# Performance work log

Measured on AMD Instinct MI355X. Metric: run time of the kernel, lower is better.

## Reference

```python
import jax, jax.numpy as jnp
import numpy as np

NB_HEADS = 12


def setup_inputs() -> dict:
    key = jax.random.key(0)
    ks = jax.random.split(key, 6)
    B, S, D, H = 4, 1024, 768, NB_HEADS
    x = jax.random.normal(ks[0], (B, S, D), dtype=jnp.float32)
    Wqkv = jax.random.normal(ks[1], (D, 3 * D), dtype=jnp.float32) * 0.02
    bqkv = jnp.zeros((3 * D,), dtype=jnp.float32)
    Wl = jax.random.normal(ks[2], (H, H), dtype=jnp.float32) * 0.3
    bl = jnp.zeros((H,), dtype=jnp.float32)
    Ww = jax.random.normal(ks[3], (H, H), dtype=jnp.float32) * 0.3
    bw = jnp.zeros((H,), dtype=jnp.float32)
    Wproj = jax.random.normal(ks[4], (D, D), dtype=jnp.float32) * 0.02
    bproj = jnp.zeros((D,), dtype=jnp.float32)
    return {"x": x, "Wqkv": Wqkv, "bqkv": bqkv, "Wl": Wl, "bl": bl,
            "Ww": Ww, "bw": bw, "Wproj": Wproj, "bproj": bproj}


def reference(x, Wqkv, bqkv, Wl, bl, Ww, bw, Wproj, bproj):
    B, S, D = x.shape
    H = NB_HEADS
    dh = D // H
    scale = dh ** (-0.5)
    # qkv projection: [B,S,3D] -> [3,B,H,S,dh]
    qkv = (x @ Wqkv + bqkv).reshape(B, S, 3, H, dh).transpose(2, 0, 3, 1, 4)
    q, k, v = qkv[0] * scale, qkv[1], qkv[2]
    # raw attention logits [B,H,S,S]
    attn = jnp.einsum('bhqd,bhkd->bhqk', q, k)
    # pre-softmax talking-heads mix across head dim (Dense over heads)
    attn = jnp.einsum('bhqk,hg->bgqk', attn, Wl) + bl[None, :, None, None]
    attn = jax.nn.softmax(attn, axis=-1)
    # post-softmax talking-heads mix
    attn = jnp.einsum('bhqk,hg->bgqk', attn, Ww) + bw[None, :, None, None]
    # attention-weighted values -> [B,S,D]
    out = jnp.einsum('bhqk,bhkd->bqhd', attn, v).reshape(B, S, D)
    return out @ Wproj + bproj
```

## Files before the change

### kernel.cpp

```cpp
#include <hip/hip_runtime.h>
#include <cstdint>

#define BB 4
#define SS 1024
#define DD 768
#define HH 12
#define DH 64

typedef unsigned short u16;
typedef unsigned int   u32;
typedef __attribute__((ext_vector_type(8))) short bf16x8;
typedef __attribute__((ext_vector_type(4))) float f32x4;

__device__ __forceinline__ u16 f2bf(float f) {
    u32 u = __float_as_uint(f);
    u += 0x7fffu + ((u >> 16) & 1u);
    return (u16)(u >> 16);
}
__device__ __forceinline__ float b2f(u32 lo16) {
    return __uint_as_float(lo16 << 16);
}

#if __has_builtin(__builtin_amdgcn_cvt_pk_bf16_f32)
__device__ __forceinline__ u32 pack2(float a, float b) {
    auto r = __builtin_amdgcn_cvt_pk_bf16_f32(a, b);
    u32 v; __builtin_memcpy(&v, &r, 4); return v;
}
#else
__device__ __forceinline__ u32 pack2(float a, float b) {
    return (u32)f2bf(a) | ((u32)f2bf(b) << 16);
}
#endif

#define ASYNC16(gp, lp) __builtin_amdgcn_global_load_lds( \
    (const __attribute__((address_space(1))) void*)(gp),  \
    (__attribute__((address_space(3))) void*)(lp), 16, 0, 0)

template<int BM_, int BN_, class Epi>
__device__ __forceinline__ void mfma_gemm(
    const u16* __restrict__ A, const u16* __restrict__ B,
    int K, int lda, int ldb, int m0, int n0, const Epi& epi)
{
    constexpr int MI = BM_ / 32;
    constexpr int NJ = BN_ / 32;
    __shared__ u16 Alds[BM_ * 32];
    __shared__ u16 Blds[BN_ * 32];

    const int tid  = threadIdx.x;
    const int wave = tid >> 6;
    const int lane = tid & 63;
    const int wr = wave >> 1, wc = wave & 1;

    const int ar = lane >> 2;
    const int ac = (lane & 3) * 8;

    f32x4 acc[MI][NJ] = {};

    for (int k0 = 0; k0 < K; k0 += 32) {
        __syncthreads();
#pragma unroll
        for (int j = 0; j < BM_ / 64; ++j) {
            const int rb = wave * (BM_ / 4) + j * 16;
            ASYNC16(A + (size_t)(m0 + rb + ar) * lda + k0 + ac, &Alds[rb * 32]);
        }
#pragma unroll
        for (int j = 0; j < BN_ / 64; ++j) {
            const int rb = wave * (BN_ / 4) + j * 16;
            ASYNC16(B + (size_t)(n0 + rb + ar) * ldb + k0 + ac, &Blds[rb * 32]);
        }
        __syncthreads();

        bf16x8 af[MI], bfr[NJ];
#pragma unroll
        for (int mi = 0; mi < MI; ++mi)
            af[mi] = *(const bf16x8*)&Alds[(wr * (BM_ / 2) + mi * 16 + (lane & 15)) * 32 + (lane >> 4) * 8];
#pragma unroll
        for (int nj = 0; nj < NJ; ++nj)
            bfr[nj] = *(const bf16x8*)&Blds[(wc * (BN_ / 2) + nj * 16 + (lane & 15)) * 32 + (lane >> 4) * 8];
#pragma unroll
        for (int mi = 0; mi < MI; ++mi)
#pragma unroll
            for (int nj = 0; nj < NJ; ++nj)
                acc[mi][nj] = __builtin_amdgcn_mfma_f32_16x16x32_bf16(
                    af[mi], bfr[nj], acc[mi][nj], 0, 0, 0);
    }

#pragma unroll
    for (int mi = 0; mi < MI; ++mi)
#pragma unroll
        for (int nj = 0; nj < NJ; ++nj)
#pragma unroll
            for (int r = 0; r < 4; ++r)
                epi(m0 + wr * (BM_ / 2) + mi * 16 + (lane >> 4) * 4 + r,
                    n0 + wc * (BN_ / 2) + nj * 16 + (lane & 15),
                    acc[mi][nj][r]);
}

#define CPAD 136

__global__ __launch_bounds__(256) void qkv_gemm_kernel(
    const u16* __restrict__ xb, const u16* __restrict__ Wt,
    const float* __restrict__ bias,
    u16* __restrict__ qb, u16* __restrict__ kb, u16* __restrict__ vb)
{
    __shared__ u16 Alds[128 * 32];
    __shared__ u16 Blds[128 * 32];
    __shared__ u16 Clds[128 * CPAD];

    const int tid  = threadIdx.x;
    const int wave = tid >> 6;
    const int lane = tid & 63;
    const int wr = wave >> 1, wc = wave & 1;
    const int ar = lane >> 2;
    const int ac = (lane & 3) * 8;
    const int m0 = blockIdx.y * 128, n0 = blockIdx.x * 128;

    f32x4 acc[4][4] = {};

    for (int k0 = 0; k0 < DD; k0 += 32) {
        __syncthreads();
#pragma unroll
        for (int j = 0; j < 2; ++j) {
            const int rb = wave * 32 + j * 16;
            ASYNC16(xb + (size_t)(m0 + rb + ar) * DD + k0 + ac, &Alds[rb * 32]);
            ASYNC16(Wt + (size_t)(n0 + rb + ar) * DD + k0 + ac, &Blds[rb * 32]);
        }
        __syncthreads();

        bf16x8 af[4], bfr[4];
#pragma unroll
        for (int mi = 0; mi < 4; ++mi)
            af[mi] = *(const bf16x8*)&Alds[(wr * 64 + mi * 16 + (lane & 15)) * 32 + (lane >> 4) * 8];
#pragma unroll
        for (int nj = 0; nj < 4; ++nj)
            bfr[nj] = *(const bf16x8*)&Blds[(wc * 64 + nj * 16 + (lane & 15)) * 32 + (lane >> 4) * 8];
#pragma unroll
        for (int mi = 0; mi < 4; ++mi)
#pragma unroll
            for (int nj = 0; nj < 4; ++nj)
                acc[mi][nj] = __builtin_amdgcn_mfma_f32_16x16x32_bf16(
                    af[mi], bfr[nj], acc[mi][nj], 0, 0, 0);
    }

    const int c  = n0 / DD;
    const int w0 = n0 - c * DD;
    const int hA = w0 >> 6;
    const float qs = (c == 0) ? 0.125f : 1.0f;
#pragma unroll
    for (int mi = 0; mi < 4; ++mi)
#pragma unroll
        for (int nj = 0; nj < 4; ++nj)
#pragma unroll
            for (int r = 0; r < 4; ++r) {
                const int row = wr * 64 + mi * 16 + (lane >> 4) * 4 + r;
                const int col = wc * 64 + nj * 16 + (lane & 15);
                Clds[row * CPAD + col] = f2bf((acc[mi][nj][r] + bias[n0 + col]) * qs);
            }
    __syncthreads();

    u16* const dst = (c == 0) ? qb : (c == 1) ? kb : vb;
    const int b = m0 >> 10;
#pragma unroll
    for (int j = 0; j < 8; ++j) {
        const int idx = j * 256 + tid;
        const int row = idx >> 4, u4 = idx & 15;
        const int half = u4 >> 3, d8 = u4 & 7;
        const int h = hA + half;
        const int s = (m0 + row) & 1023;
        const uint4 v = *(const uint4*)&Clds[row * CPAD + half * 64 + d8 * 8];
        *(uint4*)&dst[(((size_t)(b * HH + h) << 10) + s) * DH + d8 * 8] = v;
    }
}

__global__ __launch_bounds__(256) void vtrans_kernel(
    const u16* __restrict__ vb, u16* __restrict__ vt)
{
    __shared__ u16 t[64 * 72];
    const int tid = threadIdx.x;
    const int bh = blockIdx.y;
    const int s0 = blockIdx.x * 64;
    const u16* src = vb + ((size_t)bh << 16) + (size_t)s0 * DH;

#pragma unroll
    for (int j = 0; j < 2; ++j) {
        const int idx = j * 256 + tid;
        const int row = idx >> 3, u4 = idx & 7;
        *(uint4*)&t[row * 72 + u4 * 8] = *(const uint4*)&src[row * DH + u4 * 8];
    }
    __syncthreads();

#pragma unroll
    for (int j = 0; j < 2; ++j) {
        const int idx = j * 256 + tid;
        const int d = idx >> 3, u4 = idx & 7;
        u16 tmp[8];
#pragma unroll
        for (int i = 0; i < 8; ++i) tmp[i] = t[(u4 * 8 + i) * 72 + d];
        *(uint4*)&vt[((size_t)bh * DH + d) * SS + s0 + u4 * 8] = *(const uint4*)tmp;
    }
}

__global__ __launch_bounds__(256) void qk_gemm_kernel(
    const u16* __restrict__ qb, const u16* __restrict__ kb,
    u16* __restrict__ attn, int bh0)
{
    __shared__ u16 Alds[128 * 32];
    __shared__ u16 Blds[128 * 32];
    __shared__ u16 Clds[128 * CPAD];

    const int tid  = threadIdx.x;
    const int wave = tid >> 6;
    const int lane = tid & 63;
    const int wr = wave >> 1, wc = wave & 1;
    const int ar = lane >> 2;
    const int ac = (lane & 3) * 8;
    const int m0 = blockIdx.y * 128, n0 = blockIdx.x * 128;

    const int bhL = blockIdx.z;
    const u16* A = qb + (size_t)(bh0 + bhL) * SS * DH;
    const u16* B = kb + (size_t)(bh0 + bhL) * SS * DH;
    u16* C = attn + (size_t)bhL * SS * SS;

    f32x4 acc[4][4] = {};

#pragma unroll
    for (int k0 = 0; k0 < DH; k0 += 32) {
        __syncthreads();
#pragma unroll
        for (int j = 0; j < 2; ++j) {
            const int rb = wave * 32 + j * 16;
            ASYNC16(A + (size_t)(m0 + rb + ar) * DH + k0 + ac, &Alds[rb * 32]);
            ASYNC16(B + (size_t)(n0 + rb + ar) * DH + k0 + ac, &Blds[rb * 32]);
        }
        __syncthreads();

        bf16x8 af[4], bfr[4];
#pragma unroll
        for (int mi = 0; mi < 4; ++mi)
            af[mi] = *(const bf16x8*)&Alds[(wr * 64 + mi * 16 + (lane & 15)) * 32 + (lane >> 4) * 8];
#pragma unroll
        for (int nj = 0; nj < 4; ++nj)
            bfr[nj] = *(const bf16x8*)&Blds[(wc * 64 + nj * 16 + (lane & 15)) * 32 + (lane >> 4) * 8];
#pragma unroll
        for (int mi = 0; mi < 4; ++mi)
#pragma unroll
            for (int nj = 0; nj < 4; ++nj)
                acc[mi][nj] = __builtin_amdgcn_mfma_f32_16x16x32_bf16(
                    af[mi], bfr[nj], acc[mi][nj], 0, 0, 0);
    }

#pragma unroll
    for (int mi = 0; mi < 4; ++mi)
#pragma unroll
        for (int nj = 0; nj < 4; ++nj)
#pragma unroll
            for (int r = 0; r < 4; ++r) {
                const int row = wr * 64 + mi * 16 + (lane >> 4) * 4 + r;
                const int col = wc * 64 + nj * 16 + (lane & 15);
                Clds[row * CPAD + col] = f2bf(acc[mi][nj][r]);
            }
    __syncthreads();

#pragma unroll
    for (int j = 0; j < 8; ++j) {
        const int idx = j * 256 + tid;
        const int row = idx >> 4, u4 = idx & 15;
        *(uint4*)&C[(size_t)(m0 + row) * SS + n0 + u4 * 8] =
            *(const uint4*)&Clds[row * CPAD + u4 * 8];
    }
}

__global__ __launch_bounds__(256) void pv_gemm_kernel(
    const u16* __restrict__ attn2, const u16* __restrict__ vt,
    u16* __restrict__ ctx, int bh0)
{
    const int bhL = blockIdx.z;
    const int bh = bh0 + bhL;
    const int b = bh / HH, h = bh % HH;
    const u16* A = attn2 + (size_t)bhL * SS * SS;
    const u16* B = vt + (size_t)bh * DH * SS;
    u16* C = ctx + (size_t)b * SS * DD + h * DH;
    struct Epi {
        u16* C;
        __device__ void operator()(int m, int n, float v) const {
            C[(size_t)m * DD + n] = f2bf(v);
        }
    } epi{C};
    mfma_gemm<64, 64>(A, B, SS, SS, SS, blockIdx.y * 64, 0, epi);
}

__global__ __launch_bounds__(256) void proj_gemm_kernel(
    const u16* __restrict__ ctx, const u16* __restrict__ Wt,
    const float* __restrict__ bias, float* __restrict__ out)
{
    struct Epi {
        float* out; const float* bias;
        __device__ void operator()(int m, int n, float v) const {
            out[(size_t)m * DD + n] = v + bias[n];
        }
    } epi{out, bias};
    mfma_gemm<128, 64>(ctx, Wt, DD, DD, DD, blockIdx.y * 128, blockIdx.x * 64, epi);
}

__global__ __launch_bounds__(256) void mix_softmax_kernel(
    const u16* __restrict__ attn, u16* __restrict__ attn2,
    const float* __restrict__ Wl, const float* __restrict__ bl,
    const float* __restrict__ Ww, const float* __restrict__ bw)
{
    __shared__ u16 buf[HH][SS];
    __shared__ float invden[HH];

    const int tid  = threadIdx.x;
    const int wave = tid >> 6;
    const int lane = tid & 63;
    const int bL = blockIdx.x >> 10;
    const int qi = blockIdx.x & (SS - 1);
    const size_t gbase = ((size_t)bL * HH * SS + qi) * SS + tid * 4;
    const int kc = tid * 4;

#pragma unroll
    for (int h = 0; h < HH; ++h)
        *(uint2*)&buf[h][kc] = *(const uint2*)&attn[gbase + (size_t)h * SS * SS];

    {
        float4 vin[HH];
#pragma unroll
        for (int h = 0; h < HH; ++h) {
            const uint2 u = *(const uint2*)&buf[h][kc];
            vin[h].x = b2f(u.x & 0xffff); vin[h].y = b2f(u.x >> 16);
            vin[h].z = b2f(u.y & 0xffff); vin[h].w = b2f(u.y >> 16);
        }
#pragma unroll
        for (int g = 0; g < HH; ++g) {
            float4 s = {bl[g], bl[g], bl[g], bl[g]};
#pragma unroll
            for (int h = 0; h < HH; ++h) {
                const float w = Wl[h * HH + g];
                s.x += vin[h].x * w; s.y += vin[h].y * w;
                s.z += vin[h].z * w; s.w += vin[h].w * w;
            }
            uint2 p;
            p.x = pack2(s.x, s.y); p.y = pack2(s.z, s.w);
            *(uint2*)&buf[g][kc] = p;
        }
    }
    __syncthreads();

#pragma unroll
    for (int rep = 0; rep < 3; ++rep) {
        const int g = rep * 4 + wave;
        float4 v[4];
#pragma unroll
        for (int j = 0; j < 4; ++j) {
            const uint2 u = *(const uint2*)&buf[g][lane * 4 + j * 256];
            v[j].x = b2f(u.x & 0xffff); v[j].y = b2f(u.x >> 16);
            v[j].z = b2f(u.y & 0xffff); v[j].w = b2f(u.y >> 16);
        }

        float ps = 0.f;
#pragma unroll
        for (int j = 0; j < 4; ++j) {
            v[j].x = __expf(v[j].x); v[j].y = __expf(v[j].y);
            v[j].z = __expf(v[j].z); v[j].w = __expf(v[j].w);
            ps += (v[j].x + v[j].y) + (v[j].z + v[j].w);
        }
#pragma unroll
        for (int off = 32; off; off >>= 1) ps += __shfl_xor(ps, off);

#pragma unroll
        for (int j = 0; j < 4; ++j) {
            uint2 p;
            p.x = pack2(v[j].x, v[j].y); p.y = pack2(v[j].z, v[j].w);
            *(uint2*)&buf[g][lane * 4 + j * 256] = p;
        }
        if (lane == 0) invden[g] = 1.0f / ps;
    }
    __syncthreads();

    {
        float4 vin[HH];
#pragma unroll
        for (int h = 0; h < HH; ++h) {
            const uint2 u = *(const uint2*)&buf[h][kc];
            const float inv = invden[h];
            vin[h].x = b2f(u.x & 0xffff) * inv; vin[h].y = b2f(u.x >> 16) * inv;
            vin[h].z = b2f(u.y & 0xffff) * inv; vin[h].w = b2f(u.y >> 16) * inv;
        }
#pragma unroll
        for (int g = 0; g < HH; ++g) {
            float4 s = {bw[g], bw[g], bw[g], bw[g]};
#pragma unroll
            for (int h = 0; h < HH; ++h) {
                const float w = Ww[h * HH + g];
                s.x += vin[h].x * w; s.y += vin[h].y * w;
                s.z += vin[h].z * w; s.w += vin[h].w * w;
            }
            uint2 p;
            p.x = pack2(s.x, s.y); p.y = pack2(s.z, s.w);
            *(uint2*)&attn2[gbase + (size_t)g * SS * SS] = p;
        }
    }
}


__global__ __launch_bounds__(256) void cvt_bf16_kernel(
    const float* __restrict__ in, u16* __restrict__ out, int n8)
{
    const int i = blockIdx.x * 256 + threadIdx.x;
    if (i >= n8) return;
    const float4 a = ((const float4*)in)[i * 2];
    const float4 b = ((const float4*)in)[i * 2 + 1];
    uint4 p;
    p.x = pack2(a.x, a.y); p.y = pack2(a.z, a.w);
    p.z = pack2(b.x, b.y); p.w = pack2(b.z, b.w);
    ((uint4*)out)[i] = p;
}

__global__ __launch_bounds__(256) void cvt_transpose_kernel(
    const float* __restrict__ in, u16* __restrict__ out, int R, int C)
{
    __shared__ float t[32][33];
    const int c0 = blockIdx.x * 32, r0 = blockIdx.y * 32;
    const int tr = threadIdx.x >> 3;
    const int tc = (threadIdx.x & 7) * 4;
    const float4 v = *(const float4*)&in[(size_t)(r0 + tr) * C + c0 + tc];
    t[tc + 0][tr] = v.x; t[tc + 1][tr] = v.y;
    t[tc + 2][tr] = v.z; t[tc + 3][tr] = v.w;
    __syncthreads();
    uint2 p;
    p.x = pack2(t[tr][tc + 0], t[tr][tc + 1]);
    p.y = pack2(t[tr][tc + 2], t[tr][tc + 3]);
    *(uint2*)&out[(size_t)(c0 + tr) * R + r0 + tc] = p;
}

extern "C" void kernel_launch(void* const* d_in, const int* in_sizes, int n_in,
                              void* d_out, int out_size, void* d_ws, size_t ws_size,
                              hipStream_t stream)
{
    const float* x     = (const float*)d_in[0];
    const float* Wqkv  = (const float*)d_in[1];
    const float* bqkv  = (const float*)d_in[2];
    const float* Wl    = (const float*)d_in[3];
    const float* bl    = (const float*)d_in[4];
    const float* Ww    = (const float*)d_in[5];
    const float* bw    = (const float*)d_in[6];
    const float* Wproj = (const float*)d_in[7];
    const float* bproj = (const float*)d_in[8];
    float* out = (float*)d_out;

    const size_t N_XB  = (size_t)BB * SS * DD;
    const size_t N_QB  = (size_t)BB * HH * SS * DH;
    const size_t N_WT  = (size_t)DD * 3 * DD;
    const size_t N_WP  = (size_t)DD * DD;
    const size_t N_AT1 = (size_t)HH * SS * SS;

    u16* xb  = (u16*)d_ws;
    u16* qb  = xb  + N_XB;
    u16* kb  = qb  + N_QB;
    u16* vb  = kb  + N_QB;
    u16* vt  = vb  + N_QB;
    u16* ctx = vt  + N_QB;
    u16* Wqkv_t = ctx + N_XB;
    u16* Wproj_t = Wqkv_t + N_WT;
    u16* attn = Wproj_t + N_WP;

    const size_t fixed_bytes = (size_t)(N_XB * 2 + N_QB * 4 + N_WT + N_WP) * 2;
    int b_per = BB;
    while (b_per > 1 &&
           fixed_bytes + (size_t)b_per * N_AT1 * 2 * 2 > ws_size)
        b_per >>= 1;
    const int n_iter = BB / b_per;
    u16* attn2 = attn + (size_t)b_per * N_AT1;

    const dim3 blk(256);

    cvt_bf16_kernel<<<dim3((N_XB / 8 + 255) / 256), blk, 0, stream>>>(x, xb, (int)(N_XB / 8));
    cvt_transpose_kernel<<<dim3(3 * DD / 32, DD / 32), blk, 0, stream>>>(Wqkv, Wqkv_t, DD, 3 * DD);
    cvt_transpose_kernel<<<dim3(DD / 32, DD / 32), blk, 0, stream>>>(Wproj, Wproj_t, DD, DD);

    qkv_gemm_kernel<<<dim3(3 * DD / 128, BB * SS / 128), blk, 0, stream>>>(
        xb, Wqkv_t, bqkv, qb, kb, vb);
    vtrans_kernel<<<dim3(SS / 64, BB * HH), blk, 0, stream>>>(vb, vt);

    for (int it = 0; it < n_iter; ++it) {
        const int bh0 = it * b_per * HH;
        qk_gemm_kernel<<<dim3(SS / 128, SS / 128, b_per * HH), blk, 0, stream>>>(
            qb, kb, attn, bh0);
        mix_softmax_kernel<<<dim3(b_per * SS), blk, 0, stream>>>(
            attn, attn2, Wl, bl, Ww, bw);
        pv_gemm_kernel<<<dim3(1, SS / 64, b_per * HH), blk, 0, stream>>>(
            attn2, vt, ctx, bh0);
    }

    proj_gemm_kernel<<<dim3(DD / 64, BB * SS / 128), blk, 0, stream>>>(
        ctx, Wproj_t, bproj, out);
}
```

Baseline: 232.5 us.

## Use MFMA for talking-heads mixes and fold softmax normalization into weights

The two 12x12 head-mixing steps in the fused mix/softmax kernel now run as 16x16x32 bf16 MFMA instructions instead of scalar FMA loops. Exponentials are kept in registers and computed with exp2 on log2e-prescaled weights. The per-head softmax denominators are folded into the post-mix weight matrix, which removes a full LDS read/write pass. LDS rows are padded to reduce bank conflicts, at the cost of padding zeros in the MFMA operands, extra cross-lane shuffles and bf16 rounding of the scaled weights.

```diff
diff --git a/kernel.cpp b/kernel.cpp
--- a/kernel.cpp
+++ b/kernel.cpp
@@ -19,6 +19,10 @@
 }
 __device__ __forceinline__ float b2f(u32 lo16) {
     return __uint_as_float(lo16 << 16);
+}
+
+__device__ __forceinline__ float fast_exp2(float x) {
+    return __builtin_amdgcn_exp2f(x);
 }
 
 #if __has_builtin(__builtin_amdgcn_cvt_pk_bf16_f32)
@@ -302,17 +306,22 @@
     mfma_gemm<128, 64>(ctx, Wt, DD, DD, DD, blockIdx.y * 128, blockIdx.x * 64, epi);
 }
 
+#define BSTRIDE 1028
+
 __global__ __launch_bounds__(256) void mix_softmax_kernel(
     const u16* __restrict__ attn, u16* __restrict__ attn2,
     const float* __restrict__ Wl, const float* __restrict__ bl,
     const float* __restrict__ Ww, const float* __restrict__ bw)
 {
-    __shared__ u16 buf[HH][SS];
-    __shared__ float invden[HH];
+    __shared__ u16 buf[HH * BSTRIDE];
+    __shared__ float wsum[4][16];
+    __shared__ float invd[16];
 
     const int tid  = threadIdx.x;
     const int wave = tid >> 6;
     const int lane = tid & 63;
+    const int u    = lane >> 4;
+    const int ln   = lane & 15;
     const int bL = blockIdx.x >> 10;
     const int qi = blockIdx.x & (SS - 1);
     const size_t gbase = ((size_t)bL * HH * SS + qi) * SS + tid * 4;
@@ -320,86 +329,113 @@
 
 #pragma unroll
     for (int h = 0; h < HH; ++h)
-        *(uint2*)&buf[h][kc] = *(const uint2*)&attn[gbase + (size_t)h * SS * SS];
-
+        *(uint2*)&buf[h * BSTRIDE + kc] = *(const uint2*)&attn[gbase + (size_t)h * SS * SS];
+
+    bf16x8 a1;
     {
-        float4 vin[HH];
-#pragma unroll
-        for (int h = 0; h < HH; ++h) {
-            const uint2 u = *(const uint2*)&buf[h][kc];
-            vin[h].x = b2f(u.x & 0xffff); vin[h].y = b2f(u.x >> 16);
-            vin[h].z = b2f(u.y & 0xffff); vin[h].w = b2f(u.y >> 16);
-        }
-#pragma unroll
-        for (int g = 0; g < HH; ++g) {
-            float4 s = {bl[g], bl[g], bl[g], bl[g]};
-#pragma unroll
-            for (int h = 0; h < HH; ++h) {
-                const float w = Wl[h * HH + g];
-                s.x += vin[h].x * w; s.y += vin[h].y * w;
-                s.z += vin[h].z * w; s.w += vin[h].w * w;
-            }
-            uint2 p;
-            p.x = pack2(s.x, s.y); p.y = pack2(s.z, s.w);
-            *(uint2*)&buf[g][kc] = p;
-        }
-    }
-    __syncthreads();
-
-#pragma unroll
-    for (int rep = 0; rep < 3; ++rep) {
-        const int g = rep * 4 + wave;
-        float4 v[4];
-#pragma unroll
-        for (int j = 0; j < 4; ++j) {
-            const uint2 u = *(const uint2*)&buf[g][lane * 4 + j * 256];
-            v[j].x = b2f(u.x & 0xffff); v[j].y = b2f(u.x >> 16);
-            v[j].z = b2f(u.y & 0xffff); v[j].w = b2f(u.y >> 16);
-        }
-
-        float ps = 0.f;
-#pragma unroll
-        for (int j = 0; j < 4; ++j) {
-            v[j].x = __expf(v[j].x); v[j].y = __expf(v[j].y);
-            v[j].z = __expf(v[j].z); v[j].w = __expf(v[j].w);
-            ps += (v[j].x + v[j].y) + (v[j].z + v[j].w);
-        }
-#pragma unroll
-        for (int off = 32; off; off >>= 1) ps += __shfl_xor(ps, off);
-
-#pragma unroll
-        for (int j = 0; j < 4; ++j) {
-            uint2 p;
-            p.x = pack2(v[j].x, v[j].y); p.y = pack2(v[j].z, v[j].w);
-            *(uint2*)&buf[g][lane * 4 + j * 256] = p;
-        }
-        if (lane == 0) invden[g] = 1.0f / ps;
-    }
-    __syncthreads();
-
+        u16 t[8];
+#pragma unroll
+        for (int j = 0; j < 8; ++j) {
+            const int k = u * 8 + j;
+            t[j] = (k < HH && ln < HH) ? f2bf(Wl[k * HH + ln] * 1.44269504f) : (u16)0;
+        }
+        __builtin_memcpy(&a1, t, 16);
+    }
+    f32x4 c1 = {0.f, 0.f, 0.f, 0.f};
+#pragma unroll
+    for (int r = 0; r < 4; ++r) {
+        const int g = u * 4 + r;
+        c1[r] = (g < HH) ? bl[g] * 1.44269504f : 0.f;
+    }
+
+    __syncthreads();
+
+    const int posbase = wave * 256;
+
+    u32 plo[16], phi[16];
+    float part[4] = {0.f, 0.f, 0.f, 0.f};
+
+#pragma unroll
+    for (int mi = 0; mi < 16; ++mi) {
+        const int pos = posbase + mi * 16 + ln;
+        u16 t[8];
+#pragma unroll
+        for (int j = 0; j < 8; ++j) {
+            const int k = u * 8 + j;
+            t[j] = (k < HH) ? buf[k * BSTRIDE + pos] : (u16)0;
+        }
+        bf16x8 bfrag; __builtin_memcpy(&bfrag, t, 16);
+        f32x4 d = __builtin_amdgcn_mfma_f32_16x16x32_bf16(a1, bfrag, c1, 0, 0, 0);
+        const float e0 = fast_exp2(d[0]);
+        const float e1 = fast_exp2(d[1]);
+        const float e2 = fast_exp2(d[2]);
+        const float e3 = fast_exp2(d[3]);
+        part[0] += e0; part[1] += e1; part[2] += e2; part[3] += e3;
+        plo[mi] = pack2(e0, e1);
+        phi[mi] = pack2(e2, e3);
+    }
+
+#pragma unroll
+    for (int off = 1; off < 16; off <<= 1) {
+#pragma unroll
+        for (int r = 0; r < 4; ++r) part[r] += __shfl_xor(part[r], off);
+    }
+    if (ln == 0) {
+#pragma unroll
+        for (int r = 0; r < 4; ++r) wsum[wave][u * 4 + r] = part[r];
+    }
+    __syncthreads();
+    if (tid < 16)
+        invd[tid] = 1.f / (wsum[0][tid] + wsum[1][tid] + wsum[2][tid] + wsum[3][tid]);
+    __syncthreads();
+
+    bf16x8 a2;
     {
-        float4 vin[HH];
-#pragma unroll
-        for (int h = 0; h < HH; ++h) {
-            const uint2 u = *(const uint2*)&buf[h][kc];
-            const float inv = invden[h];
-            vin[h].x = b2f(u.x & 0xffff) * inv; vin[h].y = b2f(u.x >> 16) * inv;
-            vin[h].z = b2f(u.y & 0xffff) * inv; vin[h].w = b2f(u.y >> 16) * inv;
-        }
-#pragma unroll
-        for (int g = 0; g < HH; ++g) {
-            float4 s = {bw[g], bw[g], bw[g], bw[g]};
-#pragma unroll
-            for (int h = 0; h < HH; ++h) {
-                const float w = Ww[h * HH + g];
-                s.x += vin[h].x * w; s.y += vin[h].y * w;
-                s.z += vin[h].z * w; s.w += vin[h].w * w;
-            }
-            uint2 p;
-            p.x = pack2(s.x, s.y); p.y = pack2(s.z, s.w);
-            *(uint2*)&attn2[gbase + (size_t)g * SS * SS] = p;
-        }
-    }
+        u16 t[8];
+#pragma unroll
+        for (int j = 0; j < 8; ++j) {
+            const int k = u * 8 + j;
+            t[j] = (k < HH && ln < HH) ? f2bf(Ww[k * HH + ln] * invd[k]) : (u16)0;
+        }
+        __builtin_memcpy(&a2, t, 16);
+    }
+    f32x4 c2 = {0.f, 0.f, 0.f, 0.f};
+#pragma unroll
+    for (int r = 0; r < 4; ++r) {
+        const int g = u * 4 + r;
+        c2[r] = (g < HH) ? bw[g] : 0.f;
+    }
+
+    const int srcA = ln + ((u == 1) ? 32 : 16);
+#pragma unroll
+    for (int mi = 0; mi < 16; ++mi) {
+        const u32 wlo = plo[mi], whi = phi[mi];
+        const u32 slo = (u32)__shfl((int)wlo, srcA);
+        const u32 shi = (u32)__shfl((int)whi, srcA);
+        u32 wv[4];
+        wv[0] = (u == 0) ? wlo : ((u == 1) ? slo : 0u);
+        wv[1] = (u == 0) ? whi : ((u == 1) ? shi : 0u);
+        wv[2] = (u == 0) ? slo : 0u;
+        wv[3] = (u == 0) ? shi : 0u;
+        bf16x8 b2; __builtin_memcpy(&b2, wv, 16);
+        f32x4 d = __builtin_amdgcn_mfma_f32_16x16x32_bf16(a2, b2, c2, 0, 0, 0);
+
+        const int pos = posbase + mi * 16 + ln;
+        const u32 p01 = pack2(d[0], d[1]);
+        const u32 p23 = pack2(d[2], d[3]);
+        if (u < 3) {
+            buf[(u * 4 + 0) * BSTRIDE + pos] = (u16)p01;
+            buf[(u * 4 + 1) * BSTRIDE + pos] = (u16)(p01 >> 16);
+            buf[(u * 4 + 2) * BSTRIDE + pos] = (u16)p23;
+            buf[(u * 4 + 3) * BSTRIDE + pos] = (u16)(p23 >> 16);
+        }
+    }
+    __syncthreads();
+
+#pragma unroll
+    for (int g = 0; g < HH; ++g)
+        *(uint2*)&attn2[gbase + (size_t)g * SS * SS] =
+            *(const uint2*)&buf[g * BSTRIDE + kc];
 }
 
 
```

Result: slower. 255.9 us (+10.1%).

## Fuse QK GEMM with pre-softmax head mix and exp, MFMA post-mix

Applied to the files above, without the earlier changes.

Replaces the QK GEMM plus mix/softmax kernels with two kernels. The first computes all 12 heads' logits per 16x16 tile directly from global memory, applies the Wl head mix and exp2, writes head-interleaved exp values (padded to 16), and emits partial denominators. The second sums the partials, folds 1/denominator into Ww, and applies the post-softmax mix as a small MFMA before writing attn2. This removes one full round trip of the logits tensor, at the cost of a padded Pbuf layout, uncached direct global loads of Q/K, and strided 2-byte scattered stores in the second kernel.

```diff
diff --git a/kernel.cpp b/kernel.cpp
--- a/kernel.cpp
+++ b/kernel.cpp
@@ -19,6 +19,10 @@
 }
 __device__ __forceinline__ float b2f(u32 lo16) {
     return __uint_as_float(lo16 << 16);
+}
+
+__device__ __forceinline__ float fast_exp2(float x) {
+    return __builtin_amdgcn_exp2f(x);
 }
 
 #if __has_builtin(__builtin_amdgcn_cvt_pk_bf16_f32)
@@ -200,73 +204,132 @@
     }
 }
 
-__global__ __launch_bounds__(256) void qk_gemm_kernel(
+__global__ __launch_bounds__(256) void qkmix_kernel(
     const u16* __restrict__ qb, const u16* __restrict__ kb,
-    u16* __restrict__ attn, int bh0)
-{
-    __shared__ u16 Alds[128 * 32];
-    __shared__ u16 Blds[128 * 32];
-    __shared__ u16 Clds[128 * CPAD];
-
+    const float* __restrict__ Wl, const float* __restrict__ bl,
+    u16* __restrict__ Pbuf, float* __restrict__ den_part, int bh0)
+{
     const int tid  = threadIdx.x;
     const int wave = tid >> 6;
     const int lane = tid & 63;
-    const int wr = wave >> 1, wc = wave & 1;
-    const int ar = lane >> 2;
-    const int ac = (lane & 3) * 8;
-    const int m0 = blockIdx.y * 128, n0 = blockIdx.x * 128;
-
-    const int bhL = blockIdx.z;
-    const u16* A = qb + (size_t)(bh0 + bhL) * SS * DH;
-    const u16* B = kb + (size_t)(bh0 + bhL) * SS * DH;
-    u16* C = attn + (size_t)bhL * SS * SS;
-
-    f32x4 acc[4][4] = {};
-
-#pragma unroll
-    for (int k0 = 0; k0 < DH; k0 += 32) {
-        __syncthreads();
-#pragma unroll
-        for (int j = 0; j < 2; ++j) {
-            const int rb = wave * 32 + j * 16;
-            ASYNC16(A + (size_t)(m0 + rb + ar) * DH + k0 + ac, &Alds[rb * 32]);
-            ASYNC16(B + (size_t)(n0 + rb + ar) * DH + k0 + ac, &Blds[rb * 32]);
-        }
-        __syncthreads();
-
-        bf16x8 af[4], bfr[4];
-#pragma unroll
-        for (int mi = 0; mi < 4; ++mi)
-            af[mi] = *(const bf16x8*)&Alds[(wr * 64 + mi * 16 + (lane & 15)) * 32 + (lane >> 4) * 8];
-#pragma unroll
-        for (int nj = 0; nj < 4; ++nj)
-            bfr[nj] = *(const bf16x8*)&Blds[(wc * 64 + nj * 16 + (lane & 15)) * 32 + (lane >> 4) * 8];
-#pragma unroll
-        for (int mi = 0; mi < 4; ++mi)
-#pragma unroll
-            for (int nj = 0; nj < 4; ++nj)
-                acc[mi][nj] = __builtin_amdgcn_mfma_f32_16x16x32_bf16(
-                    af[mi], bfr[nj], acc[mi][nj], 0, 0, 0);
-    }
-
-#pragma unroll
-    for (int mi = 0; mi < 4; ++mi)
-#pragma unroll
-        for (int nj = 0; nj < 4; ++nj)
-#pragma unroll
-            for (int r = 0; r < 4; ++r) {
-                const int row = wr * 64 + mi * 16 + (lane >> 4) * 4 + r;
-                const int col = wc * 64 + nj * 16 + (lane & 15);
-                Clds[row * CPAD + col] = f2bf(acc[mi][nj][r]);
+    const int u    = lane >> 4;
+    const int ln   = lane & 15;
+    const int kr = blockIdx.x;
+    const int q0 = blockIdx.y * 16;
+    const int bL = blockIdx.z;
+
+    f32x4 dacc[HH] = {};
+
+    for (int kit = 0; kit < 4; ++kit) {
+        const int kc = kr * 256 + kit * 64 + wave * 16;
+        f32x4 acc[HH] = {};
+#pragma unroll
+        for (int h = 0; h < HH; ++h) {
+            const size_t hp = (size_t)(bh0 + bL * HH + h) << 16;
+#pragma unroll
+            for (int ks = 0; ks < 2; ++ks) {
+                const bf16x8 a = *(const bf16x8*)&qb[hp + (size_t)(q0 + ln) * DH + ks * 32 + u * 8];
+                const bf16x8 b = *(const bf16x8*)&kb[hp + (size_t)(kc + ln) * DH + ks * 32 + u * 8];
+                acc[h] = __builtin_amdgcn_mfma_f32_16x16x32_bf16(a, b, acc[h], 0, 0, 0);
             }
+        }
+#pragma unroll
+        for (int r = 0; r < 4; ++r) {
+            float m[HH];
+#pragma unroll
+            for (int g = 0; g < HH; ++g) {
+                float s = bl[g];
+#pragma unroll
+                for (int h = 0; h < HH; ++h) s += acc[h][r] * Wl[h * HH + g];
+                m[g] = fast_exp2(s * 1.44269504f);
+                dacc[g][r] += m[g];
+            }
+            u16* dst = Pbuf + ((size_t)(bL * SS + q0 + u * 4 + r) * SS + kc + ln) * 16;
+            uint4 pa; uint2 pb;
+            pa.x = pack2(m[0], m[1]);  pa.y = pack2(m[2], m[3]);
+            pa.z = pack2(m[4], m[5]);  pa.w = pack2(m[6], m[7]);
+            pb.x = pack2(m[8], m[9]);  pb.y = pack2(m[10], m[11]);
+            *(uint4*)dst = pa;
+            *(uint2*)(dst + 8) = pb;
+        }
+    }
+
+#pragma unroll
+    for (int off = 1; off < 16; off <<= 1)
+#pragma unroll
+        for (int g = 0; g < HH; ++g) {
+            dacc[g][0] += __shfl_xor(dacc[g][0], off);
+            dacc[g][1] += __shfl_xor(dacc[g][1], off);
+            dacc[g][2] += __shfl_xor(dacc[g][2], off);
+            dacc[g][3] += __shfl_xor(dacc[g][3], off);
+        }
+    if (ln == 0) {
+        const size_t dbase = ((size_t)(kr * 4 + wave) * gridDim.z + bL) * (SS * 16);
+#pragma unroll
+        for (int r = 0; r < 4; ++r) {
+            float* dp = den_part + dbase + (size_t)(q0 + u * 4 + r) * 16;
+            float4 v0, v1, v2;
+            v0.x = dacc[0][r]; v0.y = dacc[1][r]; v0.z = dacc[2][r];  v0.w = dacc[3][r];
+            v1.x = dacc[4][r]; v1.y = dacc[5][r]; v1.z = dacc[6][r];  v1.w = dacc[7][r];
+            v2.x = dacc[8][r]; v2.y = dacc[9][r]; v2.z = dacc[10][r]; v2.w = dacc[11][r];
+            *(float4*)dp = v0; *(float4*)(dp + 4) = v1; *(float4*)(dp + 8) = v2;
+        }
+    }
+}
+
+__global__ __launch_bounds__(256) void mix2_kernel(
+    const u16* __restrict__ Pbuf, const float* __restrict__ den_part,
+    const float* __restrict__ Ww, const float* __restrict__ bw,
+    u16* __restrict__ attn2, int nbz)
+{
+    __shared__ float denS[16];
+    const int tid  = threadIdx.x;
+    const int wave = tid >> 6;
+    const int lane = tid & 63;
+    const int u    = lane >> 4;
+    const int ln   = lane & 15;
+    const int bL = blockIdx.x >> 10;
+    const int q  = blockIdx.x & (SS - 1);
+
+    if (tid < 16) {
+        float s = 0.f;
+#pragma unroll
+        for (int p = 0; p < 16; ++p)
+            s += den_part[((size_t)p * nbz + bL) * (SS * 16) + q * 16 + tid];
+        denS[tid] = 1.0f / s;
+    }
     __syncthreads();
 
-#pragma unroll
-    for (int j = 0; j < 8; ++j) {
-        const int idx = j * 256 + tid;
-        const int row = idx >> 4, u4 = idx & 15;
-        *(uint4*)&C[(size_t)(m0 + row) * SS + n0 + u4 * 8] =
-            *(const uint4*)&Clds[row * CPAD + u4 * 8];
+    bf16x8 a2;
+    {
+        u16 t[8];
+#pragma unroll
+        for (int j = 0; j < 8; ++j) {
+            const int h = u * 8 + j;
+            t[j] = (h < HH && ln < HH) ? f2bf(Ww[h * HH + ln] * denS[h]) : (u16)0;
+        }
+        __builtin_memcpy(&a2, t, 16);
+    }
+    f32x4 c2 = {0.f, 0.f, 0.f, 0.f};
+#pragma unroll
+    for (int r = 0; r < 4; ++r) {
+        const int g = u * 4 + r;
+        c2[r] = (g < HH) ? bw[g] : 0.f;
+    }
+
+    const u16* prow = Pbuf + (size_t)(bL * SS + q) * SS * 16;
+    u16* const arow = attn2 + ((size_t)(bL * HH) << 20) + ((size_t)q << 10);
+#pragma unroll
+    for (int mi = 0; mi < 16; ++mi) {
+        const int pos = wave * 256 + mi * 16 + ln;
+        const bf16x8 bf = *(const bf16x8*)&prow[(size_t)pos * 16 + (u & 1) * 8];
+        const f32x4 d = __builtin_amdgcn_mfma_f32_16x16x32_bf16(a2, bf, c2, 0, 0, 0);
+#pragma unroll
+        for (int r = 0; r < 4; ++r) {
+            const int g = u * 4 + r;
+            if (g < HH)
+                arow[((size_t)g << 20) + pos] = f2bf(d[r]);
+        }
     }
 }
 
@@ -300,106 +363,6 @@
         }
     } epi{out, bias};
     mfma_gemm<128, 64>(ctx, Wt, DD, DD, DD, blockIdx.y * 128, blockIdx.x * 64, epi);
-}
-
-__global__ __launch_bounds__(256) void mix_softmax_kernel(
-    const u16* __restrict__ attn, u16* __restrict__ attn2,
-    const float* __restrict__ Wl, const float* __restrict__ bl,
-    const float* __restrict__ Ww, const float* __restrict__ bw)
-{
-    __shared__ u16 buf[HH][SS];
-    __shared__ float invden[HH];
-
-    const int tid  = threadIdx.x;
-    const int wave = tid >> 6;
-    const int lane = tid & 63;
-    const int bL = blockIdx.x >> 10;
-    const int qi = blockIdx.x & (SS - 1);
-    const size_t gbase = ((size_t)bL * HH * SS + qi) * SS + tid * 4;
-    const int kc = tid * 4;
-
-#pragma unroll
-    for (int h = 0; h < HH; ++h)
-        *(uint2*)&buf[h][kc] = *(const uint2*)&attn[gbase + (size_t)h * SS * SS];
-
-    {
-        float4 vin[HH];
-#pragma unroll
-        for (int h = 0; h < HH; ++h) {
-            const uint2 u = *(const uint2*)&buf[h][kc];
-            vin[h].x = b2f(u.x & 0xffff); vin[h].y = b2f(u.x >> 16);
-            vin[h].z = b2f(u.y & 0xffff); vin[h].w = b2f(u.y >> 16);
-        }
-#pragma unroll
-        for (int g = 0; g < HH; ++g) {
-            float4 s = {bl[g], bl[g], bl[g], bl[g]};
-#pragma unroll
-            for (int h = 0; h < HH; ++h) {
-                const float w = Wl[h * HH + g];
-                s.x += vin[h].x * w; s.y += vin[h].y * w;
-                s.z += vin[h].z * w; s.w += vin[h].w * w;
-            }
-            uint2 p;
-            p.x = pack2(s.x, s.y); p.y = pack2(s.z, s.w);
-            *(uint2*)&buf[g][kc] = p;
-        }
-    }
-    __syncthreads();
-
-#pragma unroll
-    for (int rep = 0; rep < 3; ++rep) {
-        const int g = rep * 4 + wave;
-        float4 v[4];
-#pragma unroll
-        for (int j = 0; j < 4; ++j) {
-            const uint2 u = *(const uint2*)&buf[g][lane * 4 + j * 256];
-            v[j].x = b2f(u.x & 0xffff); v[j].y = b2f(u.x >> 16);
-            v[j].z = b2f(u.y & 0xffff); v[j].w = b2f(u.y >> 16);
-        }
-
-        float ps = 0.f;
-#pragma unroll
-        for (int j = 0; j < 4; ++j) {
-            v[j].x = __expf(v[j].x); v[j].y = __expf(v[j].y);
-            v[j].z = __expf(v[j].z); v[j].w = __expf(v[j].w);
-            ps += (v[j].x + v[j].y) + (v[j].z + v[j].w);
-        }
-#pragma unroll
-        for (int off = 32; off; off >>= 1) ps += __shfl_xor(ps, off);
-
-#pragma unroll
-        for (int j = 0; j < 4; ++j) {
-            uint2 p;
-            p.x = pack2(v[j].x, v[j].y); p.y = pack2(v[j].z, v[j].w);
-            *(uint2*)&buf[g][lane * 4 + j * 256] = p;
-        }
-        if (lane == 0) invden[g] = 1.0f / ps;
-    }
-    __syncthreads();
-
-    {
-        float4 vin[HH];
-#pragma unroll
-        for (int h = 0; h < HH; ++h) {
-            const uint2 u = *(const uint2*)&buf[h][kc];
-            const float inv = invden[h];
-            vin[h].x = b2f(u.x & 0xffff) * inv; vin[h].y = b2f(u.x >> 16) * inv;
-            vin[h].z = b2f(u.y & 0xffff) * inv; vin[h].w = b2f(u.y >> 16) * inv;
-        }
-#pragma unroll
-        for (int g = 0; g < HH; ++g) {
-            float4 s = {bw[g], bw[g], bw[g], bw[g]};
-#pragma unroll
-            for (int h = 0; h < HH; ++h) {
-                const float w = Ww[h * HH + g];
-                s.x += vin[h].x * w; s.y += vin[h].y * w;
-                s.z += vin[h].z * w; s.w += vin[h].w * w;
-            }
-            uint2 p;
-            p.x = pack2(s.x, s.y); p.y = pack2(s.z, s.w);
-            *(uint2*)&attn2[gbase + (size_t)g * SS * SS] = p;
-        }
-    }
 }
 
 
@@ -453,6 +416,8 @@
     const size_t N_WT  = (size_t)DD * 3 * DD;
     const size_t N_WP  = (size_t)DD * DD;
     const size_t N_AT1 = (size_t)HH * SS * SS;
+    const size_t N_P   = (size_t)SS * SS * 16;
+    const size_t N_DEN = (size_t)16 * SS * 16;
 
     u16* xb  = (u16*)d_ws;
     u16* qb  = xb  + N_XB;
@@ -462,15 +427,17 @@
     u16* ctx = vt  + N_QB;
     u16* Wqkv_t = ctx + N_XB;
     u16* Wproj_t = Wqkv_t + N_WT;
-    u16* attn = Wproj_t + N_WP;
 
     const size_t fixed_bytes = (size_t)(N_XB * 2 + N_QB * 4 + N_WT + N_WP) * 2;
     int b_per = BB;
     while (b_per > 1 &&
-           fixed_bytes + (size_t)b_per * N_AT1 * 2 * 2 > ws_size)
+           fixed_bytes + (size_t)b_per * ((N_P + N_AT1) * 2 + N_DEN * 4) > ws_size)
         b_per >>= 1;
     const int n_iter = BB / b_per;
-    u16* attn2 = attn + (size_t)b_per * N_AT1;
+
+    u16* Pbuf  = Wproj_t + N_WP;
+    u16* attn2 = Pbuf + (size_t)b_per * N_P;
+    float* den_part = (float*)(attn2 + (size_t)b_per * N_AT1);
 
     const dim3 blk(256);
 
@@ -484,10 +451,10 @@
 
     for (int it = 0; it < n_iter; ++it) {
         const int bh0 = it * b_per * HH;
-        qk_gemm_kernel<<<dim3(SS / 128, SS / 128, b_per * HH), blk, 0, stream>>>(
-            qb, kb, attn, bh0);
-        mix_softmax_kernel<<<dim3(b_per * SS), blk, 0, stream>>>(
-            attn, attn2, Wl, bl, Ww, bw);
+        qkmix_kernel<<<dim3(4, SS / 16, b_per), blk, 0, stream>>>(
+            qb, kb, Wl, bl, Pbuf, den_part, bh0);
+        mix2_kernel<<<dim3(b_per * SS), blk, 0, stream>>>(
+            Pbuf, den_part, Ww, bw, attn2, b_per);
         pv_gemm_kernel<<<dim3(1, SS / 64, b_per * HH), blk, 0, stream>>>(
             attn2, vt, ctx, bh0);
     }
```

Result: slower. 325.4 us (+39.9%).
